# Performance work log

Hardware: AMD Instinct MI355X
Metric: run time of the kernel (lower is better)

The kernel has to match this reference:

```python
import jax, jax.numpy as jnp
import numpy as np

B, C, H, W = 4, 64, 128, 128
CQ = C // 8
EPS = 1e-5


def setup_inputs() -> dict:
    key = jax.random.key(0)
    ks = jax.random.split(key, 20)
    r = lambda k, shape, s=0.05: jax.random.normal(k, shape, dtype=jnp.float32) * s
    return {
        "x1": jax.random.normal(ks[0], (B, C, H, W), dtype=jnp.float32),
        "x2": jax.random.normal(ks[1], (B, C, H, W), dtype=jnp.float32),
        # 1x1 convs are plain channel matmuls: weight (out, in), bias (out,)
        "wqA": r(ks[2], (CQ, C)), "bqA": r(ks[3], (CQ,)),
        "wkA": r(ks[4], (CQ, C)), "bkA": r(ks[5], (CQ,)),
        "wvA": r(ks[6], (C, C)),  "bvA": r(ks[7], (C,)),
        "wqB": r(ks[8], (CQ, C)), "bqB": r(ks[9], (CQ,)),
        "wkB": r(ks[10], (CQ, C)), "bkB": r(ks[11], (CQ,)),
        "wvB": r(ks[12], (C, C)),  "bvB": r(ks[13], (C,)),
        "gA": r(ks[14], (1,), 0.1), "gB": r(ks[15], (1,), 0.1),
        "wp": r(ks[16], (C, C)), "bp": r(ks[17], (C,)),
        "bn_g": jnp.ones((C,), dtype=jnp.float32),
        "bn_b": jnp.zeros((C,), dtype=jnp.float32),
    }


def _conv1(x, w, b):
    # 1x1 conv over NCHW == per-pixel channel matmul
    return jnp.einsum('oi,bihw->bohw', w, x) + b[None, :, None, None]


def _axial(q, k, v):
    # criss-cross attention: for each pixel, attend over its row and column,
    # with the column (H) self-position masked to -inf, joint softmax over H+W.
    h = q.shape[2]
    eH = jnp.einsum('bciw,bcjw->biwj', q, k)            # [B,H,W,H] column scores
    eH = jnp.where(jnp.eye(h, dtype=bool)[:, None, :], -jnp.inf, eH)
    eW = jnp.einsum('bchi,bchj->bhij', q, k)            # [B,H,W,W] row scores
    att = jax.nn.softmax(jnp.concatenate([eH, eW], axis=3), axis=3)
    oH = jnp.einsum('bcjw,biwj->bciw', v, att[..., :h])
    oW = jnp.einsum('bchj,bhij->bchi', v, att[..., h:])
    return oH + oW


def _forward(x1, x2, wqA, bqA, wkA, bkA, wvA, bvA, wqB, bqB, wkB, bkB, wvB, bvB,
             gA, gB, wp, bp, bn_g, bn_b):
    # branch A: query from x2, key/value from x1
    out_A = _axial(_conv1(x2, wqA, bqA), _conv1(x1, wkA, bkA), _conv1(x1, wvA, bvA))
    # branch B: query/key/value all from x1
    out_B = _axial(_conv1(x1, wqB, bqB), _conv1(x1, wkB, bkB), _conv1(x1, wvB, bvB))
    diff = jnp.abs(out_A - out_B)
    p = jax.nn.gelu(_conv1(diff, wp, bp), approximate=False)
    # BatchNorm2d in training mode: batch statistics, biased variance
    m = p.mean(axis=(0, 2, 3), keepdims=True)
    v = ((p - m) ** 2).mean(axis=(0, 2, 3), keepdims=True)
    out = (p - m) / jnp.sqrt(v + EPS) * bn_g[None, :, None, None] + bn_b[None, :, None, None]
    return gA[0] * out_A + x1 + out, gB[0] * out_B + x2 + out


def reference(x1, x2, wqA, bqA, wkA, bkA, wvA, bvA, wqB, bqB, wkB, bkB, wvB, bvB,
              gA, gB, wp, bp, bn_g, bn_b):
    return _forward(x1, x2, wqA, bqA, wkA, bkA, wvA, bvA, wqB, bqB, wkB, bkB,
                    wvB, bvB, gA, gB, wp, bp, bn_g, bn_b)
```

## Files before the change

kernel.cpp:

```cpp
#include <hip/hip_runtime.h>


#define NE 4194304ull

typedef __attribute__((ext_vector_type(8))) short short8;
typedef __attribute__((ext_vector_type(4))) float f32x4;

#define HD __device__ __forceinline__

HD float b2f(unsigned short u) { union { unsigned int i; float f; } v; v.i = ((unsigned int)u) << 16; return v.f; }
HD unsigned short f2b(float x) {
  union { float f; unsigned int i; } v; v.f = x;
  unsigned int r = v.i + 0x7FFFu + ((v.i >> 16) & 1u);
  return (unsigned short)(r >> 16);
}

HD float erf_fast(float x) {
  const float ax = fabsf(x);
  const float t = 1.0f / (1.0f + 0.3275911f * ax);
  const float poly = ((((1.061405429f*t - 1.453152027f)*t + 1.421413741f)*t
                       - 0.284496736f)*t + 0.254829592f)*t;
  const float y = 1.0f - poly * __expf(-ax*ax);
  return copysignf(y, x);
}

HD unsigned short ldbf(const void* s0, int i, int f) {
  return f ? f2b(((const float*)s0)[i]) : ((const unsigned short*)s0)[i];
}

__global__ __launch_bounds__(256) void prelude_kernel(
    const void* x1,
    const void* wqA, const void* bqA, const void* wkA, const void* bkA,
    const void* wvA, const void* bvA, const void* wqB, const void* bqB,
    const void* wkB, const void* bkB, const void* wvB, const void* bvB,
    const void* wp, const void* bp, const void* gA, const void* gB,
    const void* bng, const void* bnb,
    int* flag, unsigned short* wout)
{
  __shared__ int s;
  if (threadIdx.x == 0) s = 0;
  __syncthreads();
  const float a = fabsf(b2f(((const unsigned short*)x1)[threadIdx.x]));
  if (a > 1000.0f) atomicOr(&s, 1);
  __syncthreads();
  const int f = s;
  if (blockIdx.x == 0 && threadIdx.x == 0) *flag = f;

  const void* srcs[18] = {wqA,bqA,wkA,bkA,wvA,bvA,wqB,bqB,wkB,bkB,wvB,bvB,wp,bp,gA,gB,bng,bnb};
  const int   ns[18]   = {512,  8,512,  8,4096, 64,512,  8,512,  8,4096, 64,4096,64, 1, 1, 64, 64};
  unsigned short* wqkv = wout + 14696;
  float* wbias = (float*)(wout + 25960);

  const int gstride = gridDim.x * 256;
  for (int idx = blockIdx.x*256 + threadIdx.x; idx < 26136; idx += gstride) {
    if (idx < 14690) {
      int off = idx, k2 = 0;
      while (off >= ns[k2]) { off -= ns[k2]; ++k2; }
      wout[idx] = ldbf(srcs[k2], off, f);
    } else if (idx >= 25960) {
      const int i3 = idx - 25960, mt = i3 >> 4, r = i3 & 15;
      float val = 0.0f;
      if (mt == 0)      { if (r < 8) val = b2f(ldbf(bqA, r, f)); }
      else if (mt == 1) { val = b2f((r < 8) ? ldbf(bkA, r, f) : ldbf(bqB, r - 8, f)); }
      else if (mt == 2) { if (r < 8) val = b2f(ldbf(bkB, r, f)); }
      else if (mt < 7)  { val = b2f(ldbf(bvA, (mt-3)*16 + r, f)); }
      else              { val = b2f(ldbf(bvB, (mt-7)*16 + r, f)); }
      wbias[i3] = val;
    } else if (idx >= 14696) {
      const int i2 = idx - 14696;
      const int mt = i2 >> 10, rem = i2 & 1023, r = rem >> 6, ci = rem & 63;
      unsigned short val = 0;
      if (mt == 0)      { if (r < 8) val = ldbf(wqA, r*64 + ci, f); }
      else if (mt == 1) { val = (r < 8) ? ldbf(wkA, r*64 + ci, f) : ldbf(wqB, (r-8)*64 + ci, f); }
      else if (mt == 2) { if (r < 8) val = ldbf(wkB, r*64 + ci, f); }
      else if (mt < 7)  { val = ldbf(wvA, ((mt-3)*16 + r)*64 + ci, f); }
      else              { val = ldbf(wvB, ((mt-7)*16 + r)*64 + ci, f); }
      wqkv[i2] = val;
    }
  }
}

__global__ __launch_bounds__(256) void qkv_kernel(
    const void* __restrict__ x1v, const void* __restrict__ x2v, const int* __restrict__ flag,
    const unsigned short* __restrict__ wqkv, const float* __restrict__ wbias,
    unsigned short* __restrict__ q, unsigned short* __restrict__ k,
    unsigned short* __restrict__ v)
{
  const int hp = blockIdx.x, b = blockIdx.y;
  const int h0 = hp*2;
  const int tid = threadIdx.x, lane = tid & 63, w4 = tid >> 6;
  const int col = lane & 15, quad = lane >> 4;
  const int f32m = *flag;
  __shared__ __align__(16) char smem[33792];
  unsigned short* Xb = (unsigned short*)smem;
  unsigned short* S0 = (unsigned short*)smem;
  unsigned short* S1 = (unsigned short*)(smem + 8448);
  const size_t gb = (size_t)b*1048576 + (size_t)h0*128;

  short8 Bc[2][8];
  #pragma unroll
  for (int pass = 0; pass < 2; ++pass) {
    const void* xv = pass ? x2v : x1v;
    for (int t = tid; t < 2048; t += 256) {
      const int c = t >> 5, rem = t & 31, hh = rem >> 4, w8 = (rem & 15)*8;
      const int n = hh*128 + w8;
      const size_t a = gb + (size_t)c*16384 + (size_t)hh*128 + w8;
      unsigned short vals[8];
      if (f32m) {
        const float* xf = (const float*)xv;
        const float4 f0 = *(const float4*)(xf + a);
        const float4 f1 = *(const float4*)(xf + a + 4);
        vals[0]=f2b(f0.x); vals[1]=f2b(f0.y); vals[2]=f2b(f0.z); vals[3]=f2b(f0.w);
        vals[4]=f2b(f1.x); vals[5]=f2b(f1.y); vals[6]=f2b(f1.z); vals[7]=f2b(f1.w);
      } else {
        const uint4 u = *(const uint4*)((const unsigned short*)xv + a);
        vals[0]=(unsigned short)(u.x & 0xffff); vals[1]=(unsigned short)(u.x >> 16);
        vals[2]=(unsigned short)(u.y & 0xffff); vals[3]=(unsigned short)(u.y >> 16);
        vals[4]=(unsigned short)(u.z & 0xffff); vals[5]=(unsigned short)(u.z >> 16);
        vals[6]=(unsigned short)(u.w & 0xffff); vals[7]=(unsigned short)(u.w >> 16);
      }
      #pragma unroll
      for (int i = 0; i < 8; ++i) Xb[(n + i)*66 + c] = vals[i];
    }
    __syncthreads();
    const unsigned int* U = (const unsigned int*)Xb;
    #pragma unroll
    for (int nt = 0; nt < 4; ++nt)
      #pragma unroll
      for (int ks = 0; ks < 2; ++ks) {
        const int n = w4*64 + nt*16 + col;
        const int base = n*33 + (ks*32 + quad*8)/2;
        union { unsigned int u32[4]; short8 s; } p;
        #pragma unroll
        for (int jj = 0; jj < 4; ++jj) p.u32[jj] = U[base + jj];
        Bc[pass][nt*2 + ks] = p.s;
      }
    __syncthreads();
  }

  #pragma unroll
  for (int mt = 0; mt < 11; ++mt) {
    f32x4 acc[4];
    #pragma unroll
    for (int nt = 0; nt < 4; ++nt) acc[nt] = (f32x4){0.f, 0.f, 0.f, 0.f};
    #pragma unroll
    for (int ks = 0; ks < 2; ++ks) {
      union { uint4 u; short8 s; } A;
      A.u = *(const uint4*)(wqkv + mt*1024 + col*64 + ks*32 + quad*8);
      #pragma unroll
      for (int nt = 0; nt < 4; ++nt)
        acc[nt] = __builtin_amdgcn_mfma_f32_16x16x32_bf16(
            A.s, (mt == 0) ? Bc[1][nt*2 + ks] : Bc[0][nt*2 + ks], acc[nt], 0, 0, 0);
    }
    float bias[4];
    #pragma unroll
    for (int r = 0; r < 4; ++r) bias[r] = wbias[mt*16 + quad*4 + r];
    unsigned short* S = (mt & 1) ? S1 : S0;
    #pragma unroll
    for (int nt = 0; nt < 4; ++nt)
      #pragma unroll
      for (int r = 0; r < 4; ++r) {
        const int row = quad*4 + r;
        const int nloc = w4*64 + nt*16 + col;
        S[row*264 + nloc] = f2b(acc[nt][r] + bias[r]);
      }
    __syncthreads();
    if (mt < 3) {
      const int nloc = tid;
      const int pixg = h0*128 + nloc;
      union { unsigned short u[8]; uint4 v4; } P;
      #pragma unroll
      for (int r = 0; r < 8; ++r) P.u[r] = S[r*264 + nloc];
      if (mt == 0) {
        *(uint4*)(q + ((size_t)b*16384 + pixg)*8) = P.v4;
      } else if (mt == 1) {
        *(uint4*)(k + ((size_t)b*16384 + pixg)*8) = P.v4;
        #pragma unroll
        for (int r = 0; r < 8; ++r) P.u[r] = S[(8 + r)*264 + nloc];
        *(uint4*)(q + ((size_t)(4 + b)*16384 + pixg)*8) = P.v4;
      } else {
        *(uint4*)(k + ((size_t)(4 + b)*16384 + pixg)*8) = P.v4;
      }
    } else {
      const int vm = (mt >= 7) ? mt - 7 : mt - 3;
      const int z  = (mt >= 7) ? 4 + b : b;
      const int cl = tid >> 4, u = tid & 15;
      const int co = vm*16 + cl;
      const uint4 a0 = *(const uint4*)&S[cl*264 + u*16];
      const uint4 a1 = *(const uint4*)&S[cl*264 + u*16 + 8];
      unsigned short* dst = v + ((size_t)(z*64 + co)*16384 + (size_t)h0*128 + u*16);
      *(uint4*)dst = a0;
      *(uint4*)(dst + 8) = a1;
    }
  }
}

__global__ __launch_bounds__(256) void transpose_v(
    const unsigned short* __restrict__ vStd, unsigned short* __restrict__ vT)
{
  const int tile = blockIdx.x, c = blockIdx.y, z = blockIdx.z;
  const int h0 = (tile & 3) * 32, w0 = (tile >> 2) * 32;
  const size_t base = ((size_t)z*64 + c) * 16384;
  __shared__ unsigned short T[32][33];
  const int tid = threadIdx.x;
  for (int idx = tid; idx < 1024; idx += 256) {
    const int r = idx >> 5, cc = idx & 31;
    T[r][cc] = vStd[base + (size_t)(h0 + r)*128 + (w0 + cc)];
  }
  __syncthreads();
  for (int idx = tid; idx < 1024; idx += 256) {
    const int r = idx >> 5, cc = idx & 31;
    vT[base + (size_t)(w0 + r)*128 + (h0 + cc)] = T[cc][r];
  }
}

__global__ __launch_bounds__(256) void pv_kernel(
    const unsigned short* __restrict__ q, const unsigned short* __restrict__ k,
    const unsigned short* __restrict__ vStd, const unsigned short* __restrict__ vT,
    unsigned short* __restrict__ outBrH, unsigned short* __restrict__ oColH,
    float* __restrict__ lRow, float* __restrict__ lCol)
{
  const int X = blockIdx.x, b = blockIdx.y;
  const int br = blockIdx.z & 1, dir = blockIdx.z >> 1;
  const int tid = threadIdx.x, lane = tid & 63, w4 = tid >> 6;
  const int col = lane & 15, quad = lane >> 4;
  const int z = br*4 + b;
  const size_t b4h = (size_t)z * 128;
  __shared__ __align__(16) char smemA[34048];
  __shared__ __align__(16) char smemB[16384];
  unsigned short* P = (unsigned short*)smemA;
  float* Dst = (float*)smemA;
  uint4* Ks = (uint4*)smemB;
  uint4* Vl = (uint4*)smemB;

  if (tid < 128) {
    const int j = tid;
    const size_t pix = (b4h + (dir ? X : j))*128 + (dir ? j : X);
    Ks[j] = *(const uint4*)(k + pix*8);
  }
  __syncthreads();

  const uint4 zero4 = {0u, 0u, 0u, 0u};
  short8 Afr[2];
  #pragma unroll
  for (int ib2 = 0; ib2 < 2; ++ib2) {
    uint4 a = zero4;
    if (quad == 0) {
      const int m = (w4*2 + ib2)*16 + col;
      const size_t pix = (b4h + (dir ? X : m))*128 + (dir ? m : X);
      a = *(const uint4*)(q + pix*8);
    }
    union { uint4 u; short8 s; } cv; cv.u = a; Afr[ib2] = cv.s;
  }
  float lsum[2][4];
  #pragma unroll
  for (int ib2 = 0; ib2 < 2; ++ib2)
    #pragma unroll
    for (int r = 0; r < 4; ++r) lsum[ib2][r] = 0.0f;
  #pragma unroll
  for (int nb = 0; nb < 8; ++nb) {
    uint4 bu = (quad == 0) ? Ks[nb*16 + col] : zero4;
    union { uint4 u; short8 s; } bv; bv.u = bu;
    f32x4 sA = __builtin_amdgcn_mfma_f32_16x16x32_bf16(Afr[0], bv.s, (f32x4){0.f,0.f,0.f,0.f}, 0, 0, 0);
    f32x4 sB = __builtin_amdgcn_mfma_f32_16x16x32_bf16(Afr[1], bv.s, (f32x4){0.f,0.f,0.f,0.f}, 0, 0, 0);
    const int j = nb*16 + col;
    #pragma unroll
    for (int ib2 = 0; ib2 < 2; ++ib2) {
      const int mbase = (w4*2 + ib2)*16 + quad*4;
      #pragma unroll
      for (int r = 0; r < 4; ++r) {
        const int m = mbase + r;
        const float sv = ib2 ? sB[r] : sA[r];
        float p = 0.0f;
        if (dir || (j != m)) p = __expf(sv);
        lsum[ib2][r] += p;
        P[m*132 + j] = f2b(p);
      }
    }
  }
  #pragma unroll
  for (int ib2 = 0; ib2 < 2; ++ib2)
    #pragma unroll
    for (int r = 0; r < 4; ++r) {
      float s = lsum[ib2][r];
      s += __shfl_xor(s, 1); s += __shfl_xor(s, 2);
      s += __shfl_xor(s, 4); s += __shfl_xor(s, 8);
      if (col == 0) {
        const int m = (w4*2 + ib2)*16 + quad*4 + r;
        float* lOut = dir ? lRow : lCol;
        lOut[((size_t)z*128 + X)*128 + m] = s;
      }
    }
  __syncthreads();

  short8 af[2][4];
  #pragma unroll
  for (int ib2 = 0; ib2 < 2; ++ib2) {
    const int m = (w4*2 + ib2)*16 + col;
    #pragma unroll
    for (int kb = 0; kb < 4; ++kb) {
      const int j0 = kb*32 + quad*8;
      union { uint2 u[2]; short8 s; } pk;
      pk.u[0] = *(const uint2*)&P[m*132 + j0];
      pk.u[1] = *(const uint2*)&P[m*132 + j0 + 4];
      af[ib2][kb] = pk.s;
    }
  }
  const unsigned short* vsrc = dir ? vStd : vT;
  const size_t vbase = ((size_t)z*64)*16384 + (size_t)X*128;
  for (int t = tid; t < 1024; t += 256) {
    const int vl = t & 63, nb = (t >> 6) & 3, kb = t >> 8;
    const int c = nb*16 + (vl & 15), j0 = kb*32 + ((vl >> 4) << 3);
    Vl[t] = *(const uint4*)(vsrc + vbase + (size_t)c*16384 + j0);
  }
  __syncthreads();

  f32x4 acc[2][4];
  #pragma unroll
  for (int i2 = 0; i2 < 2; ++i2)
    #pragma unroll
    for (int nb = 0; nb < 4; ++nb) acc[i2][nb] = (f32x4){0.f, 0.f, 0.f, 0.f};
  #pragma unroll
  for (int nb = 0; nb < 4; ++nb)
    #pragma unroll
    for (int kb = 0; kb < 4; ++kb) {
      const short8 bfr = *(short8*)&Vl[(kb*4 + nb)*64 + lane];
      acc[0][nb] = __builtin_amdgcn_mfma_f32_16x16x32_bf16(af[0][kb], bfr, acc[0][nb], 0, 0, 0);
      acc[1][nb] = __builtin_amdgcn_mfma_f32_16x16x32_bf16(af[1][kb], bfr, acc[1][nb], 0, 0, 0);
    }
  __syncthreads();

  #pragma unroll
  for (int i2 = 0; i2 < 2; ++i2)
    #pragma unroll
    for (int nb = 0; nb < 4; ++nb)
      #pragma unroll
      for (int r = 0; r < 4; ++r) {
        const int mm = (w4*2 + i2)*16 + ((lane >> 4) << 2) + r;
        const int cc = nb*16 + (lane & 15);
        Dst[cc*133 + mm] = acc[i2][nb][r];
      }
  __syncthreads();
  unsigned short* dsth = dir ? outBrH : oColH;
  for (int t = tid; t < 2048; t += 256) {
    const int cc = t >> 5, mm4 = (t & 31) * 4;
    const float* sp = &Dst[cc*133 + mm4];
    uint2 u;
    u.x = (unsigned int)f2b(sp[0]) | ((unsigned int)f2b(sp[1]) << 16);
    u.y = (unsigned int)f2b(sp[2]) | ((unsigned int)f2b(sp[3]) << 16);
    *(uint2*)(dsth + vbase + (size_t)cc*16384 + mm4) = u;
  }
}

__global__ __launch_bounds__(256) void combine_kernel(
    const unsigned short* __restrict__ oColU, const float* __restrict__ lRow,
    const float* __restrict__ lCol, unsigned short* __restrict__ outBr)
{
  const int tile = blockIdx.x, z = blockIdx.y, cg = blockIdx.z;
  const int h0 = (tile & 3) * 32, w0 = (tile >> 2) * 32, c0 = cg*8;
  const int tid = threadIdx.x;
  __shared__ float Tl[32][33];
  __shared__ __align__(16) float inv[32][36];
  __shared__ __align__(16) float T4[4][32][36];
  const size_t lzb = (size_t)z * 16384;
  {
    const int w = tid >> 3, h4 = (tid & 7)*4;
    const float4 vc = *(const float4*)(lCol + lzb + (size_t)(w0 + w)*128 + h0 + h4);
    Tl[w][h4+0] = vc.x; Tl[w][h4+1] = vc.y; Tl[w][h4+2] = vc.z; Tl[w][h4+3] = vc.w;
  }
  __syncthreads();
  {
    const int h = tid >> 3, w4 = (tid & 7)*4;
    const float4 lr = *(const float4*)(lRow + lzb + (size_t)(h0 + h)*128 + w0 + w4);
    float4 iv;
    iv.x = 1.0f / (lr.x + Tl[w4+0][h]);
    iv.y = 1.0f / (lr.y + Tl[w4+1][h]);
    iv.z = 1.0f / (lr.z + Tl[w4+2][h]);
    iv.w = 1.0f / (lr.w + Tl[w4+3][h]);
    *(float4*)&inv[h][w4] = iv;
  }
  __syncthreads();
  #pragma unroll
  for (int half = 0; half < 2; ++half) {
    for (int t = tid; t < 1024; t += 256) {
      const int ch = t >> 8, rem = t & 255, w = rem >> 3, h4 = (rem & 7)*4;
      const int c = c0 + half*4 + ch;
      const uint2 vc = *(const uint2*)(oColU + ((size_t)(z*64 + c))*16384
                                       + (size_t)(w0 + w)*128 + h0 + h4);
      float4 f;
      f.x = b2f((unsigned short)(vc.x & 0xffff)); f.y = b2f((unsigned short)(vc.x >> 16));
      f.z = b2f((unsigned short)(vc.y & 0xffff)); f.w = b2f((unsigned short)(vc.y >> 16));
      *(float4*)&T4[ch][w][h4] = f;
    }
    __syncthreads();
    for (int t = tid; t < 1024; t += 256) {
      const int ch = t >> 8, rem = t & 255, h = rem >> 3, w4 = (rem & 7)*4;
      const int c = c0 + half*4 + ch;
      const size_t off = ((size_t)(z*64 + c))*16384 + (size_t)(h0 + h)*128 + w0 + w4;
      const uint2 ov = *(const uint2*)(outBr + off);
      const float4 iv = *(const float4*)&inv[h][w4];
      float o0 = b2f((unsigned short)(ov.x & 0xffff));
      float o1 = b2f((unsigned short)(ov.x >> 16));
      float o2 = b2f((unsigned short)(ov.y & 0xffff));
      float o3 = b2f((unsigned short)(ov.y >> 16));
      o0 = (o0 + T4[ch][w4+0][h]) * iv.x;
      o1 = (o1 + T4[ch][w4+1][h]) * iv.y;
      o2 = (o2 + T4[ch][w4+2][h]) * iv.z;
      o3 = (o3 + T4[ch][w4+3][h]) * iv.w;
      uint2 u;
      u.x = (unsigned int)f2b(o0) | ((unsigned int)f2b(o1) << 16);
      u.y = (unsigned int)f2b(o2) | ((unsigned int)f2b(o3) << 16);
      *(uint2*)(outBr + off) = u;
    }
    __syncthreads();
  }
}

__global__ __launch_bounds__(256) void proj_kernel(
    const unsigned short* __restrict__ outA, const unsigned short* __restrict__ outB,
    const unsigned short* __restrict__ wp, const unsigned short* __restrict__ bp,
    float* __restrict__ pbuf, float* __restrict__ part)
{
  const int hp = blockIdx.x, b = blockIdx.y;
  const int tid = threadIdx.x, lane = tid & 63, w4 = tid >> 6;
  const int col = lane & 15, quad = lane >> 4;
  __shared__ __align__(16) char smem[17408];
  unsigned short* Xb = (unsigned short*)smem;
  float* S = (float*)smem;

  const size_t gb = (size_t)b*1048576 + (size_t)hp*64;
  for (int t = tid; t < 512; t += 256) {
    const int c = t >> 3, rem = t & 7;
    const size_t a = gb + (size_t)c*16384 + rem*8;
    const uint4 ua = *(const uint4*)(outA + a);
    const uint4 ub = *(const uint4*)(outB + a);
    const unsigned short* pa = (const unsigned short*)&ua;
    const unsigned short* pb = (const unsigned short*)&ub;
    const int n = rem*8;
    #pragma unroll
    for (int i = 0; i < 8; ++i)
      Xb[(n + i)*66 + c] = f2b(fabsf(b2f(pa[i]) - b2f(pb[i])));
  }
  __syncthreads();

  short8 Bc[8];
  const unsigned int* U = (const unsigned int*)Xb;
  #pragma unroll
  for (int nt = 0; nt < 4; ++nt)
    #pragma unroll
    for (int ks = 0; ks < 2; ++ks) {
      const int n = nt*16 + col;
      const int base = n*33 + (ks*32 + quad*8)/2;
      union { unsigned int u32[4]; short8 s; } p;
      #pragma unroll
      for (int jj = 0; jj < 4; ++jj) p.u32[jj] = U[base + jj];
      Bc[nt*2 + ks] = p.s;
    }
  __syncthreads();

  f32x4 acc[4];
  #pragma unroll
  for (int nt = 0; nt < 4; ++nt) acc[nt] = (f32x4){0.f, 0.f, 0.f, 0.f};
  #pragma unroll
  for (int ks = 0; ks < 2; ++ks) {
    union { uint4 u; short8 s; } A;
    A.u = *(const uint4*)(wp + (w4*16 + col)*64 + ks*32 + quad*8);
    #pragma unroll
    for (int nt = 0; nt < 4; ++nt)
      acc[nt] = __builtin_amdgcn_mfma_f32_16x16x32_bf16(A.s, Bc[nt*2 + ks], acc[nt], 0, 0, 0);
  }

  float sg1[4] = {0.f, 0.f, 0.f, 0.f}, sg2[4] = {0.f, 0.f, 0.f, 0.f};
  #pragma unroll
  for (int nt = 0; nt < 4; ++nt)
    #pragma unroll
    for (int r = 0; r < 4; ++r) {
      const float x = acc[nt][r] + b2f(bp[w4*16 + quad*4 + r]);
      const float g = 0.5f * x * (1.0f + erf_fast(x * 0.70710678118f));
      S[(w4*16 + quad*4 + r)*68 + nt*16 + col] = g;
      sg1[r] += g; sg2[r] += g*g;
    }
  const int slot = hp*4 + b;
  #pragma unroll
  for (int r = 0; r < 4; ++r) {
    float s1 = sg1[r], s2 = sg2[r];
    s1 += __shfl_xor(s1, 1); s1 += __shfl_xor(s1, 2);
    s1 += __shfl_xor(s1, 4); s1 += __shfl_xor(s1, 8);
    s2 += __shfl_xor(s2, 1); s2 += __shfl_xor(s2, 2);
    s2 += __shfl_xor(s2, 4); s2 += __shfl_xor(s2, 8);
    if (col == 0) {
      const int co = w4*16 + quad*4 + r;
      part[(size_t)co*1024 + slot] = s1;
      part[(size_t)(64 + co)*1024 + slot] = s2;
    }
  }
  __syncthreads();

  for (int t = tid; t < 1024; t += 256) {
    const int row = t >> 4, px4 = (t & 15)*4;
    const float4 v4 = *(const float4*)&S[row*68 + px4];
    *(float4*)(pbuf + (size_t)(b*64 + row)*16384 + hp*64 + px4) = v4;
  }
}

__global__ __launch_bounds__(256) void reduce_kernel(
    const float* __restrict__ part, float* __restrict__ bnAcc)
{
  const int stat = blockIdx.x, tid = threadIdx.x;
  const float4 v = *(const float4*)(part + (size_t)stat*1024 + tid*4);
  float s = v.x + v.y + v.z + v.w;
  #pragma unroll
  for (int off = 32; off >= 1; off >>= 1) s += __shfl_xor(s, off);
  __shared__ float ws4[4];
  if ((tid & 63) == 0) ws4[tid >> 6] = s;
  __syncthreads();
  if (tid == 0) bnAcc[stat] = ws4[0] + ws4[1] + ws4[2] + ws4[3];
}

__global__ __launch_bounds__(256) void final_kernel(
    const float* __restrict__ pbuf,
    const unsigned short* __restrict__ outAH, const unsigned short* __restrict__ outBH,
    const void* __restrict__ x1v, const void* __restrict__ x2v, const int* __restrict__ flag,
    const unsigned short* __restrict__ gA, const unsigned short* __restrict__ gB,
    const unsigned short* __restrict__ bng, const unsigned short* __restrict__ bnb,
    const float* __restrict__ bnAcc, void* __restrict__ outv)
{
  const int f32m = *flag;
  const int idx = (blockIdx.x * 256 + threadIdx.x) * 4;
  const int c = (idx >> 14) & 63;
  const float invN = 1.0f / 65536.0f;
  const float s1 = bnAcc[c], s2 = bnAcc[64 + c];
  const float mean = s1 * invN;
  const float var = s2 * invN - mean*mean;
  const float scale = rsqrtf(var + 1e-5f) * b2f(bng[c]);
  const float beta = b2f(bnb[c]);
  const float ga = b2f(gA[0]), gb = b2f(gB[0]);
  const float4 p4 = *(const float4*)(pbuf + idx);
  const uint2 uA = *(const uint2*)(outAH + idx);
  const uint2 uB = *(const uint2*)(outBH + idx);
  float p[4] = {p4.x, p4.y, p4.z, p4.w};
  float a[4] = { b2f((unsigned short)(uA.x & 0xffff)), b2f((unsigned short)(uA.x >> 16)),
                 b2f((unsigned short)(uA.y & 0xffff)), b2f((unsigned short)(uA.y >> 16)) };
  float bb[4] = { b2f((unsigned short)(uB.x & 0xffff)), b2f((unsigned short)(uB.x >> 16)),
                  b2f((unsigned short)(uB.y & 0xffff)), b2f((unsigned short)(uB.y >> 16)) };
  float xa[4], xb[4];
  if (f32m) {
    const float4 t1 = *(const float4*)((const float*)x1v + idx);
    const float4 t2 = *(const float4*)((const float*)x2v + idx);
    xa[0]=t1.x; xa[1]=t1.y; xa[2]=t1.z; xa[3]=t1.w;
    xb[0]=t2.x; xb[1]=t2.y; xb[2]=t2.z; xb[3]=t2.w;
  } else {
    const uint2 x1u = *(const uint2*)((const unsigned short*)x1v + idx);
    const uint2 x2u = *(const uint2*)((const unsigned short*)x2v + idx);
    xa[0] = b2f((unsigned short)(x1u.x & 0xffff)); xa[1] = b2f((unsigned short)(x1u.x >> 16));
    xa[2] = b2f((unsigned short)(x1u.y & 0xffff)); xa[3] = b2f((unsigned short)(x1u.y >> 16));
    xb[0] = b2f((unsigned short)(x2u.x & 0xffff)); xb[1] = b2f((unsigned short)(x2u.x >> 16));
    xb[2] = b2f((unsigned short)(x2u.y & 0xffff)); xb[3] = b2f((unsigned short)(x2u.y >> 16));
  }
  float o1f[4], o2f[4];
  #pragma unroll
  for (int t = 0; t < 4; ++t) {
    const float nv = (p[t] - mean)*scale + beta;
    o1f[t] = ga*a[t] + xa[t] + nv;
    o2f[t] = gb*bb[t] + xb[t] + nv;
  }
  if (f32m) {
    float* of = (float*)outv;
    *(float4*)(of + idx)      = (float4){o1f[0], o1f[1], o1f[2], o1f[3]};
    *(float4*)(of + NE + idx) = (float4){o2f[0], o2f[1], o2f[2], o2f[3]};
  } else {
    unsigned short* oh = (unsigned short*)outv;
    uint2 u1, u2;
    u1.x = (unsigned int)f2b(o1f[0]) | ((unsigned int)f2b(o1f[1]) << 16);
    u1.y = (unsigned int)f2b(o1f[2]) | ((unsigned int)f2b(o1f[3]) << 16);
    u2.x = (unsigned int)f2b(o2f[0]) | ((unsigned int)f2b(o2f[1]) << 16);
    u2.y = (unsigned int)f2b(o2f[2]) | ((unsigned int)f2b(o2f[3]) << 16);
    *(uint2*)(oh + idx) = u1;
    *(uint2*)(oh + NE + idx) = u2;
  }
}

extern "C" void kernel_launch(void* const* d_in, const int* in_sizes, int n_in,
                              void* d_out, int out_size, void* d_ws, size_t ws_size,
                              hipStream_t stream)
{
  const void* x1  = d_in[0];
  const void* x2  = d_in[1];

  char* ws = (char*)d_ws;
  const size_t MB = 1048576ull;
  unsigned short* q     = (unsigned short*)(ws);
  unsigned short* kk    = (unsigned short*)(ws + 2*MB);
  float* lRow           = (float*)(ws + 4*MB);
  float* lCol           = (float*)(ws + 4*MB + 512*1024);
  unsigned short* vStd  = (unsigned short*)(ws + 6*MB);
  unsigned short* vT    = (unsigned short*)(ws + 22*MB);
  unsigned short* outBrH= (unsigned short*)(ws + 38*MB);
  unsigned short* oColH = (unsigned short*)(ws + 54*MB);
  float* pbuf           = (float*)(ws + 70*MB);
  float* part           = (float*)(ws + 86*MB);
  float* bnAcc          = (float*)(ws + 102*MB);
  int*   flag           = (int*)(ws + 102*MB + 512);
  unsigned short* wC    = (unsigned short*)(ws + 102*MB + 1024);

  prelude_kernel<<<64, 256, 0, stream>>>(
      x1, d_in[2], d_in[3], d_in[4], d_in[5], d_in[6], d_in[7], d_in[8], d_in[9],
      d_in[10], d_in[11], d_in[12], d_in[13], d_in[16], d_in[17], d_in[14], d_in[15],
      d_in[18], d_in[19], flag, wC);
  qkv_kernel<<<dim3(64, 4), 256, 0, stream>>>(
      x1, x2, flag, wC + 14696, (const float*)(wC + 25960), q, kk, vStd);
  transpose_v<<<dim3(16, 64, 8), 256, 0, stream>>>(vStd, vT);
  pv_kernel<<<dim3(128, 4, 4), 256, 0, stream>>>(q, kk, vStd, vT, outBrH, oColH, lRow, lCol);
  combine_kernel<<<dim3(16, 8, 8), 256, 0, stream>>>(oColH, lRow, lCol, outBrH);
  proj_kernel<<<dim3(256, 4), 256, 0, stream>>>(outBrH, outBrH + NE, wC + 10400, wC + 14496, pbuf, part);
  reduce_kernel<<<128, 256, 0, stream>>>(part, bnAcc);
  final_kernel<<<4096, 256, 0, stream>>>(pbuf, outBrH, outBrH + NE, x1, x2, flag,
                                         wC + 14560, wC + 14561, wC + 14562, wC + 14626,
                                         bnAcc, d_out);
}
```

Baseline: 216.2 us.

## Restructure pv_kernel with 32x32 MFMA, register-resident P and swizzled LDS

Rewrites the attention-PV kernel to use 32x32x16 bf16 MFMAs, computing transposed scores (K·Q) so the exp'd probabilities stay in registers. They are repacked into A-fragments with cross-half-wave shuffles instead of a round trip through shared memory. V tiles and the bf16 output staging use an XOR-swizzled 16KB LDS buffer instead of padded arrays, cutting LDS from about 50KB to 16KB. A launch-bounds occupancy hint of 4 blocks is added. The risks are register pressure from the packed P arrays and subtle fragment-layout errors in the shuffle-based repacking.

```diff
diff --git a/kernel.cpp b/kernel.cpp
--- a/kernel.cpp
+++ b/kernel.cpp
@@ -5,6 +5,7 @@
 
 typedef __attribute__((ext_vector_type(8))) short short8;
 typedef __attribute__((ext_vector_type(4))) float f32x4;
+typedef __attribute__((ext_vector_type(16))) float f32x16;
 
 #define HD __device__ __forceinline__
 
@@ -13,6 +14,9 @@
   union { float f; unsigned int i; } v; v.f = x;
   unsigned int r = v.i + 0x7FFFu + ((v.i >> 16) & 1u);
   return (unsigned short)(r >> 16);
+}
+HD unsigned int pk2(float a, float b) {
+  return (unsigned int)f2b(a) | ((unsigned int)f2b(b) << 16);
 }
 
 HD float erf_fast(float x) {
@@ -214,7 +218,7 @@
   }
 }
 
-__global__ __launch_bounds__(256) void pv_kernel(
+__global__ __launch_bounds__(256, 4) void pv_kernel(
     const unsigned short* __restrict__ q, const unsigned short* __restrict__ k,
     const unsigned short* __restrict__ vStd, const unsigned short* __restrict__ vT,
     unsigned short* __restrict__ outBrH, unsigned short* __restrict__ oColH,
@@ -223,132 +227,126 @@
   const int X = blockIdx.x, b = blockIdx.y;
   const int br = blockIdx.z & 1, dir = blockIdx.z >> 1;
   const int tid = threadIdx.x, lane = tid & 63, w4 = tid >> 6;
-  const int col = lane & 15, quad = lane >> 4;
+  const int lm = lane & 31, l5 = lane >> 5;
   const int z = br*4 + b;
   const size_t b4h = (size_t)z * 128;
-  __shared__ __align__(16) char smemA[34048];
-  __shared__ __align__(16) char smemB[16384];
-  unsigned short* P = (unsigned short*)smemA;
-  float* Dst = (float*)smemA;
-  uint4* Ks = (uint4*)smemB;
-  uint4* Vl = (uint4*)smemB;
-
-  if (tid < 128) {
-    const int j = tid;
-    const size_t pix = (b4h + (dir ? X : j))*128 + (dir ? j : X);
-    Ks[j] = *(const uint4*)(k + pix*8);
-  }
-  __syncthreads();
-
-  const uint4 zero4 = {0u, 0u, 0u, 0u};
-  short8 Afr[2];
-  #pragma unroll
-  for (int ib2 = 0; ib2 < 2; ++ib2) {
-    uint4 a = zero4;
-    if (quad == 0) {
-      const int m = (w4*2 + ib2)*16 + col;
-      const size_t pix = (b4h + (dir ? X : m))*128 + (dir ? m : X);
-      a = *(const uint4*)(q + pix*8);
-    }
-    union { uint4 u; short8 s; } cv; cv.u = a; Afr[ib2] = cv.s;
-  }
-  float lsum[2][4];
-  #pragma unroll
-  for (int ib2 = 0; ib2 < 2; ++ib2)
-    #pragma unroll
-    for (int r = 0; r < 4; ++r) lsum[ib2][r] = 0.0f;
-  #pragma unroll
-  for (int nb = 0; nb < 8; ++nb) {
-    uint4 bu = (quad == 0) ? Ks[nb*16 + col] : zero4;
-    union { uint4 u; short8 s; } bv; bv.u = bu;
-    f32x4 sA = __builtin_amdgcn_mfma_f32_16x16x32_bf16(Afr[0], bv.s, (f32x4){0.f,0.f,0.f,0.f}, 0, 0, 0);
-    f32x4 sB = __builtin_amdgcn_mfma_f32_16x16x32_bf16(Afr[1], bv.s, (f32x4){0.f,0.f,0.f,0.f}, 0, 0, 0);
-    const int j = nb*16 + col;
-    #pragma unroll
-    for (int ib2 = 0; ib2 < 2; ++ib2) {
-      const int mbase = (w4*2 + ib2)*16 + quad*4;
-      #pragma unroll
-      for (int r = 0; r < 4; ++r) {
-        const int m = mbase + r;
-        const float sv = ib2 ? sB[r] : sA[r];
-        float p = 0.0f;
-        if (dir || (j != m)) p = __expf(sv);
-        lsum[ib2][r] += p;
-        P[m*132 + j] = f2b(p);
-      }
-    }
-  }
-  #pragma unroll
-  for (int ib2 = 0; ib2 < 2; ++ib2)
-    #pragma unroll
-    for (int r = 0; r < 4; ++r) {
-      float s = lsum[ib2][r];
-      s += __shfl_xor(s, 1); s += __shfl_xor(s, 2);
-      s += __shfl_xor(s, 4); s += __shfl_xor(s, 8);
-      if (col == 0) {
-        const int m = (w4*2 + ib2)*16 + quad*4 + r;
-        float* lOut = dir ? lRow : lCol;
-        lOut[((size_t)z*128 + X)*128 + m] = s;
-      }
-    }
-  __syncthreads();
-
-  short8 af[2][4];
-  #pragma unroll
-  for (int ib2 = 0; ib2 < 2; ++ib2) {
-    const int m = (w4*2 + ib2)*16 + col;
-    #pragma unroll
-    for (int kb = 0; kb < 4; ++kb) {
-      const int j0 = kb*32 + quad*8;
-      union { uint2 u[2]; short8 s; } pk;
-      pk.u[0] = *(const uint2*)&P[m*132 + j0];
-      pk.u[1] = *(const uint2*)&P[m*132 + j0 + 4];
-      af[ib2][kb] = pk.s;
-    }
-  }
+  __shared__ __align__(16) char smem[16384];
+
   const unsigned short* vsrc = dir ? vStd : vT;
   const size_t vbase = ((size_t)z*64)*16384 + (size_t)X*128;
   for (int t = tid; t < 1024; t += 256) {
-    const int vl = t & 63, nb = (t >> 6) & 3, kb = t >> 8;
-    const int c = nb*16 + (vl & 15), j0 = kb*32 + ((vl >> 4) << 3);
-    Vl[t] = *(const uint4*)(vsrc + vbase + (size_t)c*16384 + j0);
-  }
-  __syncthreads();
-
-  f32x4 acc[2][4];
-  #pragma unroll
-  for (int i2 = 0; i2 < 2; ++i2)
-    #pragma unroll
-    for (int nb = 0; nb < 4; ++nb) acc[i2][nb] = (f32x4){0.f, 0.f, 0.f, 0.f};
-  #pragma unroll
-  for (int nb = 0; nb < 4; ++nb)
-    #pragma unroll
-    for (int kb = 0; kb < 4; ++kb) {
-      const short8 bfr = *(short8*)&Vl[(kb*4 + nb)*64 + lane];
-      acc[0][nb] = __builtin_amdgcn_mfma_f32_16x16x32_bf16(af[0][kb], bfr, acc[0][nb], 0, 0, 0);
-      acc[1][nb] = __builtin_amdgcn_mfma_f32_16x16x32_bf16(af[1][kb], bfr, acc[1][nb], 0, 0, 0);
-    }
-  __syncthreads();
-
-  #pragma unroll
-  for (int i2 = 0; i2 < 2; ++i2)
-    #pragma unroll
-    for (int nb = 0; nb < 4; ++nb)
+    const int c = t >> 4, slot = t & 15;
+    const uint4 d = *(const uint4*)(vsrc + vbase + (size_t)c*16384 + slot*8);
+    *(uint4*)(smem + c*256 + ((slot*16) ^ ((c & 15) << 4))) = d;
+  }
+
+  const uint4 zero4 = {0u, 0u, 0u, 0u};
+  short8 kfr[4], qfr;
+  {
+    union { uint4 u; short8 s; } cv;
+    uint4 a = zero4;
+    if (l5 == 0) {
+      const int m = w4*32 + lm;
+      const size_t pix = (b4h + (dir ? X : m))*128 + (dir ? m : X);
+      a = *(const uint4*)(q + pix*8);
+    }
+    cv.u = a; qfr = cv.s;
+    #pragma unroll
+    for (int jt = 0; jt < 4; ++jt) {
+      uint4 e = zero4;
+      if (l5 == 0) {
+        const int j = jt*32 + lm;
+        const size_t pix = (b4h + (dir ? X : j))*128 + (dir ? j : X);
+        e = *(const uint4*)(k + pix*8);
+      }
+      cv.u = e; kfr[jt] = cv.s;
+    }
+  }
+
+  float lsum = 0.0f;
+  unsigned int pka[4][4], pkb[4][4];
+  #pragma unroll
+  for (int jt = 0; jt < 4; ++jt) {
+    f32x16 sacc = (f32x16){0.f,0.f,0.f,0.f,0.f,0.f,0.f,0.f,
+                           0.f,0.f,0.f,0.f,0.f,0.f,0.f,0.f};
+    sacc = __builtin_amdgcn_mfma_f32_32x32x16_bf16(kfr[jt], qfr, sacc, 0, 0, 0);
+    #pragma unroll
+    for (int r2 = 0; r2 < 4; ++r2) {
+      float pv4[4];
       #pragma unroll
-      for (int r = 0; r < 4; ++r) {
-        const int mm = (w4*2 + i2)*16 + ((lane >> 4) << 2) + r;
-        const int cc = nb*16 + (lane & 15);
-        Dst[cc*133 + mm] = acc[i2][nb][r];
+      for (int e = 0; e < 4; ++e) {
+        const int jl = e + 8*r2 + 4*l5;
+        float p = 0.0f;
+        if (dir || (jt != w4) || (jl != lm)) p = __expf(sacc[r2*4 + e]);
+        lsum += p;
+        pv4[e] = p;
       }
-  __syncthreads();
+      pka[jt][r2] = pk2(pv4[0], pv4[1]);
+      pkb[jt][r2] = pk2(pv4[2], pv4[3]);
+    }
+  }
+
+  lsum += __shfl_xor(lsum, 32);
+  if (l5 == 0) {
+    float* lOut = dir ? lRow : lCol;
+    lOut[((size_t)z*128 + X)*128 + w4*32 + lm] = lsum;
+  }
+
+  short8 af[8];
+  #pragma unroll
+  for (int kb = 0; kb < 8; ++kb) {
+    const int qq = kb & 1, jt = kb >> 1;
+    const unsigned int ownA = l5 ? pka[jt][2*qq+1] : pka[jt][2*qq];
+    const unsigned int ownB = l5 ? pkb[jt][2*qq+1] : pkb[jt][2*qq];
+    const unsigned int sndA = l5 ? pka[jt][2*qq]   : pka[jt][2*qq+1];
+    const unsigned int sndB = l5 ? pkb[jt][2*qq]   : pkb[jt][2*qq+1];
+    const unsigned int rcvA = (unsigned int)__shfl_xor((int)sndA, 32);
+    const unsigned int rcvB = (unsigned int)__shfl_xor((int)sndB, 32);
+    union { unsigned int u[4]; short8 s; } t4;
+    t4.u[0] = l5 ? rcvA : ownA;
+    t4.u[1] = l5 ? rcvB : ownB;
+    t4.u[2] = l5 ? ownA : rcvA;
+    t4.u[3] = l5 ? ownB : rcvB;
+    af[kb] = t4.s;
+  }
+
+  __syncthreads();
+
+  f32x16 acc[2];
+  acc[0] = (f32x16){0.f,0.f,0.f,0.f,0.f,0.f,0.f,0.f,0.f,0.f,0.f,0.f,0.f,0.f,0.f,0.f};
+  acc[1] = acc[0];
+  #pragma unroll
+  for (int kb = 0; kb < 8; ++kb) {
+    #pragma unroll
+    for (int nb = 0; nb < 2; ++nb) {
+      const int c = nb*32 + lm;
+      union { uint4 u; short8 s; } bv;
+      bv.u = *(const uint4*)(smem + c*256 + (((kb*2 + l5)*16) ^ ((c & 15) << 4)));
+      acc[nb] = __builtin_amdgcn_mfma_f32_32x32x16_bf16(af[kb], bv.s, acc[nb], 0, 0, 0);
+    }
+  }
+
+  __syncthreads();
+
+  #pragma unroll
+  for (int nb = 0; nb < 2; ++nb) {
+    const int c = nb*32 + lm;
+    #pragma unroll
+    for (int r2 = 0; r2 < 4; ++r2) {
+      uint2 u;
+      u.x = pk2(acc[nb][r2*4+0], acc[nb][r2*4+1]);
+      u.y = pk2(acc[nb][r2*4+2], acc[nb][r2*4+3]);
+      const int mbyte = w4*64 + r2*16 + l5*8;
+      *(uint2*)(smem + c*256 + (mbyte ^ ((c & 15) << 3))) = u;
+    }
+  }
+  __syncthreads();
+
   unsigned short* dsth = dir ? outBrH : oColH;
   for (int t = tid; t < 2048; t += 256) {
-    const int cc = t >> 5, mm4 = (t & 31) * 4;
-    const float* sp = &Dst[cc*133 + mm4];
-    uint2 u;
-    u.x = (unsigned int)f2b(sp[0]) | ((unsigned int)f2b(sp[1]) << 16);
-    u.y = (unsigned int)f2b(sp[2]) | ((unsigned int)f2b(sp[3]) << 16);
-    *(uint2*)(dsth + vbase + (size_t)cc*16384 + mm4) = u;
+    const int c = t >> 5, mc = t & 31;
+    const uint2 u = *(const uint2*)(smem + c*256 + ((mc*8) ^ ((c & 15) << 3)));
+    *(uint2*)(dsth + vbase + (size_t)c*16384 + mc*4) = u;
   }
 }
 
```

Result: no change. 215.1 us (-0.5%).
